# Optimization experiments

Measured on AMD Instinct MI355X. Metric: run time of the kernel, lower is better.

## Reference

```python
import jax, jax.numpy as jnp
import numpy as np

HID, FFN, E, K = 1024, 4096, 8, 2
CAP_FACTOR = 1.25


def setup_inputs() -> dict:
    key = jax.random.key(0)
    k1, k2, k3, k4 = jax.random.split(key, 4)
    B, T = 4, 2048
    x = jax.random.normal(k1, (B, T, HID), dtype=jnp.float32)
    router_w = jax.random.normal(k2, (E, HID), dtype=jnp.float32) * 0.02
    w1 = jax.random.normal(k3, (E, HID, FFN), dtype=jnp.float32) * 0.02
    w2 = jax.random.normal(k4, (E, FFN, HID), dtype=jnp.float32) * 0.02
    return {"x": x, "router_w": router_w, "w1": w1, "w2": w2}


def reference(x, router_w, w1, w2):
    B, T, H = x.shape
    N = B * T
    x_flat = x.reshape(N, H)
    # capacity per expert (static, shape-derived)
    C = max(1, int(CAP_FACTOR * N / E * K))

    # router (eval mode: no noise)
    logits = x_flat @ router_w.T                      # [N, E]
    probs = jax.nn.softmax(logits, axis=-1)
    top_v, top_i = jax.lax.top_k(probs, K)            # [N, K]
    top_v = top_v / jnp.sum(top_v, axis=-1, keepdims=True)

    out = jnp.zeros_like(x_flat)
    for k in range(K):
        eid = top_i[:, k]                             # [N] expert id per token
        gate = top_v[:, k]                            # [N]
        # position of each token within its expert, in token order
        onehot = jax.nn.one_hot(eid, E, dtype=jnp.int32)          # [N, E]
        pos = jnp.take_along_axis(jnp.cumsum(onehot, axis=0), eid[:, None], axis=1)[:, 0] - 1
        keep = pos < C                                # capacity drop (first C in token order)
        slot = jnp.where(keep, eid * C + pos, E * C)  # dropped tokens -> dump slot

        # dispatch: scatter kept tokens into per-expert capacity buffers
        buf = jnp.zeros((E * C + 1, H), dtype=x.dtype).at[slot].add(
            x_flat * keep[:, None].astype(x.dtype))
        expert_in = buf[: E * C].reshape(E, C, H)     # [E, C, H]

        # per-expert FFN (grouped GEMM -> GELU -> grouped GEMM)
        h = jax.nn.gelu(jnp.einsum('ech,ehf->ecf', expert_in, w1), approximate=False)
        y = jnp.einsum('ecf,efh->ech', h, w2)         # [E, C, H]

        # combine: gather back to token order, mask dropped, apply gate
        tok = y.reshape(E * C, H)[jnp.minimum(slot, E * C - 1)]
        out = out + tok * (gate * keep.astype(x.dtype))[:, None]

    return out.reshape(B, T, H)
```

## Files before the change

kernel.cpp:

```cpp
#include <hip/hip_runtime.h>
#include <hip/hip_bf16.h>
#include <math.h>

#define N_TOK 8192
#define HIDD  1024
#define FFND  4096
#define NE    8
#define CAP   2560
#define TMX   20
#define RMAX  16512

typedef __attribute__((ext_vector_type(4))) float  f32x4;
typedef __attribute__((ext_vector_type(8))) __bf16 bf16x8;

__device__ __forceinline__ unsigned short f2bf(float f) {
    unsigned u = __float_as_uint(f);
    u = (u + 0x7fffu + ((u >> 16) & 1u)) >> 16;
    return (unsigned short)u;
}

__device__ __forceinline__ void gld_lds16(const void* g, void* l) {
    __builtin_amdgcn_global_load_lds(
        (const __attribute__((address_space(1))) unsigned int*)g,
        (__attribute__((address_space(3))) unsigned int*)l, 16, 0, 0);
}

template <int R, int C>
__global__ __launch_bounds__(256) void transpose_cvt(const float* __restrict__ W,
                                                     unsigned short* __restrict__ Wt) {
    __shared__ unsigned short st[64][72];
    int e  = blockIdx.z;
    int r0 = blockIdx.y * 64, c0 = blockIdx.x * 64;
    int tid = threadIdx.x;
    int rb = tid >> 4, cq = tid & 15;
    const float* src = W + ((size_t)e * R + r0) * C + c0;
#pragma unroll
    for (int i = 0; i < 4; i++) {
        int kr = i * 16 + rb;
        float4 v = *reinterpret_cast<const float4*>(src + (size_t)kr * C + cq * 4);
        st[cq * 4 + 0][kr] = f2bf(v.x);
        st[cq * 4 + 1][kr] = f2bf(v.y);
        st[cq * 4 + 2][kr] = f2bf(v.z);
        st[cq * 4 + 3][kr] = f2bf(v.w);
    }
    __syncthreads();
    unsigned short* dst = Wt + ((size_t)e * C + c0) * R + r0;
#pragma unroll
    for (int i = 0; i < 4; i++) {
        int cr = i * 16 + rb;
        uint2 v = *reinterpret_cast<const uint2*>(&st[cr][cq * 4]);
        *reinterpret_cast<uint2*>(dst + (size_t)cr * R + cq * 4) = v;
    }
}

__global__ __launch_bounds__(256) void router_kernel(const float* __restrict__ x,
                                                     const float* __restrict__ rw,
                                                     unsigned short* __restrict__ xbf,
                                                     int* __restrict__ cnt,
                                                     int* __restrict__ tok,
                                                     float* __restrict__ gate) {
    __shared__ float4 rwl[2048];
    __shared__ int   e0s[32], e1s[32];
    __shared__ float g0s[32], g1s[32];
    __shared__ int   baseS[16];

    int tid = threadIdx.x, lane = tid & 63, w = tid >> 6;
    for (int i = tid; i < 2048; i += 256) rwl[i] = reinterpret_cast<const float4*>(rw)[i];
    __syncthreads();

    int tbase = blockIdx.x * 32 + w * 8;
    for (int i = 0; i < 8; i++) {
        int t = tbase + i;
        const float4* xr = reinterpret_cast<const float4*>(x) + (size_t)t * 256;
        float4 xv[4];
#pragma unroll
        for (int c = 0; c < 4; c++) xv[c] = xr[c * 64 + lane];
        uint2* xb = reinterpret_cast<uint2*>(xbf) + (size_t)t * 256;
#pragma unroll
        for (int c = 0; c < 4; c++) {
            uint2 p;
            p.x = (unsigned)f2bf(xv[c].x) | ((unsigned)f2bf(xv[c].y) << 16);
            p.y = (unsigned)f2bf(xv[c].z) | ((unsigned)f2bf(xv[c].w) << 16);
            xb[c * 64 + lane] = p;
        }
        float dot[NE];
#pragma unroll
        for (int e = 0; e < NE; e++) {
            float s = 0.f;
#pragma unroll
            for (int c = 0; c < 4; c++) {
                float4 a = rwl[e * 256 + c * 64 + lane];
                s += xv[c].x * a.x + xv[c].y * a.y + xv[c].z * a.z + xv[c].w * a.w;
            }
            dot[e] = s;
        }
#pragma unroll
        for (int e = 0; e < NE; e++) {
            float v = dot[e];
#pragma unroll
            for (int o = 32; o > 0; o >>= 1) v += __shfl_xor(v, o, 64);
            dot[e] = v;
        }
        if (lane == 0) {
            int e0 = 0; float l0 = dot[0];
#pragma unroll
            for (int e = 1; e < NE; e++) if (dot[e] > l0) { l0 = dot[e]; e0 = e; }
            int e1 = -1; float l1 = -3.4e38f;
#pragma unroll
            for (int e = 0; e < NE; e++) if (e != e0 && dot[e] > l1) { l1 = dot[e]; e1 = e; }
            float g0 = 1.f / (1.f + expf(l1 - l0));
            int j = w * 8 + i;
            e0s[j] = e0; e1s[j] = e1; g0s[j] = g0; g1s[j] = 1.f - g0;
        }
    }
    __syncthreads();

    int e0 = 255, e1 = 255, rank0 = 0, rank1 = 0, slotcnt = 0;
    float g0 = 0.f, g1 = 0.f;
    if (w == 0) {
        if (lane < 32) { e0 = e0s[lane]; e1 = e1s[lane]; g0 = g0s[lane]; g1 = g1s[lane]; }
        unsigned long long lt = (1ull << lane) - 1ull;
#pragma unroll
        for (int ee = 0; ee < NE; ee++) {
            unsigned long long m0 = __ballot(e0 == ee);
            unsigned long long m1 = __ballot(e1 == ee);
            if (e0 == ee) rank0 = (int)__popcll(m0 & lt);
            if (e1 == ee) rank1 = (int)__popcll(m1 & lt);
            if (lane == ee)      slotcnt = (int)__popcll(m0);
            if (lane == NE + ee) slotcnt = (int)__popcll(m1);
        }
        if (lane < 16) baseS[lane] = atomicAdd(&cnt[lane * 16], slotcnt);
    }
    __syncthreads();
    if (w == 0 && lane < 32) {
        int t = blockIdx.x * 32 + lane;
        int p0 = baseS[e0] + rank0;
        if (p0 < CAP) { tok[e0 * CAP + p0] = t; gate[e0 * CAP + p0] = g0; }
        int p1 = baseS[NE + e1] + rank1;
        if (p1 < CAP) { tok[(NE + e1) * CAP + p1] = t; gate[(NE + e1) * CAP + p1] = g1; }
    }
}

template <int KD, int ND, int KS, bool G1>
__global__ __launch_bounds__(512, 2) void ffn_gemm8(const unsigned short* __restrict__ A,
                                                    const unsigned short* __restrict__ Bw,
                                                    unsigned short* __restrict__ H,
                                                    float* __restrict__ O,
                                                    const int* __restrict__ cntAll,
                                                    const int* __restrict__ tokL,
                                                    const float* __restrict__ gateL) {
    constexpr int TN    = ND / 128;
    constexpr int UNITS = TN * KS;
    constexpr int CH    = G1 ? 8 : 4;
    constexpr int KDS   = KD / KS;
    constexpr int NT    = KDS / 64;
    constexpr int LDSA  = 256 * 128;
    constexpr int LDSB  = 128 * 128;
    constexpr int BUF   = LDSA + LDSB;

    extern __shared__ __align__(16) char smem[];

    int e = blockIdx.x & 7;
    int i = blockIdx.x >> 3;
    int cnt0 = min(cntAll[e * 16], CAP);
    int cnt1 = min(cntAll[(e + 8) * 16], CAP);
    int tmx0 = (cnt0 + 255) >> 8, tmx1 = (cnt1 + 255) >> 8;
    int tmsum = tmx0 + tmx1;
    if (tmsum == 0) return;
    int per_chunk = tmsum * CH;
    int c = i / per_chunk;
    if (c >= UNITS / CH) return;
    int r = i - c * per_chunk;
    int s, tm, cnt_e;
    if (r < tmx0 * CH) { s = e;     tm = r / CH; r -= tm * CH; cnt_e = cnt0; }
    else { r -= tmx0 * CH; s = e + 8; tm = r / CH; r -= tm * CH; cnt_e = cnt1; }
    int u  = c * CH + r;
    int tn = (KS > 1) ? (u / KS) : u;
    int ks = (KS > 1) ? (u % KS) : 0;

    int off_e = 0;
#pragma unroll
    for (int t = 0; t < 16; t++) off_e += (t < s) ? min(cntAll[t * 16], CAP) : 0;
    const int lbase = s * CAP;

    int tid = threadIdx.x;
    int l = tid & 63, w = tid >> 6;

    int srow = w * 8 + (l >> 3);
    int swz  = (((l & 7) ^ ((l >> 3) & 7)) << 4);

    int aoff[4];
#pragma unroll
    for (int j = 0; j < 4; j++) {
        int p = tm * 256 + j * 64 + srow;
        if (G1) {
            int t = tokL[lbase + (p < cnt_e ? p : 0)];
            aoff[j] = t * (KD * 2) + ks * (KDS * 2) + swz;
        } else {
            aoff[j] = (off_e + p) * (KD * 2) + ks * (KDS * 2) + swz;
        }
    }
    int boff[2];
#pragma unroll
    for (int j = 0; j < 2; j++) {
        int nr = e * ND + tn * 128 + j * 64 + srow;
        boff[j] = nr * (KD * 2) + ks * (KDS * 2) + swz;
    }
    int adst = w * 1024;

    const char* Ab = (const char*)A;
    const char* Bb = (const char*)Bw;

    int wm = w >> 1, wn = w & 1;
    int arow = wm * 64 + (l & 15);
    int brow = wn * 64 + (l & 15);
    int rsw  = (((l >> 4) ^ (l & 7)) << 4);
    int aR0 = arow * 128 + rsw;
    int bR0 = brow * 128 + rsw;

    f32x4 acc[4][4];
#pragma unroll
    for (int m = 0; m < 4; m++)
#pragma unroll
        for (int n = 0; n < 4; n++) acc[m][n] = (f32x4){0.f, 0.f, 0.f, 0.f};

    char* b0 = smem;
    char* b1 = smem + BUF;
    char* b2 = smem + 2 * BUF;

#define STAGE_A(buf) do { _Pragma("unroll") \
    for (int j = 0; j < 4; j++) { gld_lds16(Ab + aoff[j], (buf) + adst + j * 8192); aoff[j] += 128; } } while (0)
#define STAGE_B(buf) do { _Pragma("unroll") \
    for (int j = 0; j < 2; j++) { gld_lds16(Bb + boff[j], (buf) + LDSA + adst + j * 8192); boff[j] += 128; } } while (0)

    STAGE_A(b0); STAGE_B(b0);
    STAGE_A(b1); STAGE_B(b1);
    asm volatile("s_waitcnt vmcnt(6)" ::: "memory");
    __builtin_amdgcn_s_barrier();
    asm volatile("" ::: "memory");

    for (int t = 0; t < NT; t++) {
        bool pf = (t + 2 < NT);
        bf16x8 af[4], bf[4];
#pragma unroll
        for (int m = 0; m < 4; m++) af[m] = *reinterpret_cast<const bf16x8*>(b0 + aR0 + m * 2048);
#pragma unroll
        for (int n = 0; n < 4; n++) bf[n] = *reinterpret_cast<const bf16x8*>(b0 + LDSA + bR0 + n * 2048);
        if (pf) STAGE_A(b2);
        __builtin_amdgcn_s_setprio(1);
#pragma unroll
        for (int m = 0; m < 4; m++)
#pragma unroll
            for (int n = 0; n < 4; n++)
                acc[m][n] = __builtin_amdgcn_mfma_f32_16x16x32_bf16(af[m], bf[n], acc[m][n], 0, 0, 0);
        __builtin_amdgcn_s_setprio(0);
#pragma unroll
        for (int m = 0; m < 4; m++) af[m] = *reinterpret_cast<const bf16x8*>(b0 + (aR0 ^ 64) + m * 2048);
#pragma unroll
        for (int n = 0; n < 4; n++) bf[n] = *reinterpret_cast<const bf16x8*>(b0 + LDSA + (bR0 ^ 64) + n * 2048);
        if (pf) STAGE_B(b2);
        __builtin_amdgcn_s_setprio(1);
#pragma unroll
        for (int m = 0; m < 4; m++)
#pragma unroll
            for (int n = 0; n < 4; n++)
                acc[m][n] = __builtin_amdgcn_mfma_f32_16x16x32_bf16(af[m], bf[n], acc[m][n], 0, 0, 0);
        __builtin_amdgcn_s_setprio(0);
        if (pf) asm volatile("s_waitcnt vmcnt(6)" ::: "memory");
        else    asm volatile("s_waitcnt vmcnt(0)" ::: "memory");
        if (t + 1 < NT) {
            __builtin_amdgcn_s_barrier();
            asm volatile("" ::: "memory");
        }
        char* bt = b0; b0 = b1; b1 = b2; b2 = bt;
    }
#undef STAGE_A
#undef STAGE_B

    if (G1) {
#pragma unroll
        for (int m = 0; m < 4; m++) {
#pragma unroll
            for (int j = 0; j < 4; j++) {
                int rr = wm * 64 + m * 16 + (l >> 4) * 4 + j;
                int p = tm * 256 + rr;
                if (p < cnt_e) {
                    unsigned short* hp = H + (size_t)(off_e + p) * ND + tn * 128 + wn * 64 + (l & 15);
#pragma unroll
                    for (int n = 0; n < 4; n++) {
                        float v = acc[m][n][j];
                        float g = 0.5f * v * (1.f + erff(v * 0.70710678118654752f));
                        hp[n * 16] = f2bf(g);
                    }
                }
            }
        }
    } else {
#pragma unroll
        for (int m = 0; m < 4; m++) {
#pragma unroll
            for (int j = 0; j < 4; j++) {
                int rr = wm * 64 + m * 16 + (l >> 4) * 4 + j;
                int p = tm * 256 + rr;
                if (p < cnt_e) {
                    int t = tokL[lbase + p];
                    float gv = gateL[lbase + p];
                    float* op = O + (size_t)t * ND + tn * 128 + wn * 64 + (l & 15);
#pragma unroll
                    for (int n = 0; n < 4; n++) atomicAdd(op + n * 16, gv * acc[m][n][j]);
                }
            }
        }
    }
}

template <int KD, int ND, bool G1>
__global__ __launch_bounds__(256) void ffn_gemm(const unsigned short* __restrict__ A,
                                                const float* __restrict__ W,
                                                unsigned short* __restrict__ H,
                                                float* __restrict__ O,
                                                const int* __restrict__ cntAll,
                                                const int* __restrict__ tokL,
                                                const float* __restrict__ gateL,
                                                int slot0, int pbase) {
    constexpr int TN = ND / 128;
    int bid = blockIdx.x;
    int tn  = bid % TN;
    int tme = bid / TN;
    int tm  = tme % TMX;
    int s   = slot0 + tme / TMX;
    int eW  = s & 7;
    int cnt_e = min(cntAll[s * 16], CAP);
    if (tm * 128 >= cnt_e) return;
    int off_e = 0;
#pragma unroll
    for (int i = 0; i < 16; i++) {
        int c = min(cntAll[i * 16], CAP);
        off_e += (i >= pbase && i < s) ? c : 0;
    }
    const int lbase = s * CAP;

    __shared__ __align__(16) unsigned short At[128 * 32];
    __shared__ __align__(16) unsigned short Bt[128 * 32];

    int tid = threadIdx.x;
    int w = tid >> 6, l = tid & 63;
    int wr = w >> 1, wc = w & 1;

    int r1 = tid >> 2, q1 = tid & 3;
    int r2 = r1 + 64;
    const char* aSrc1;
    const char* aSrc2;
    if (G1) {
        int p1 = tm * 128 + r1, p2 = tm * 128 + r2;
        int t1 = tokL[lbase + (p1 < cnt_e ? p1 : 0)];
        int t2 = tokL[lbase + (p2 < cnt_e ? p2 : 0)];
        aSrc1 = (const char*)(A + (size_t)t1 * KD) + ((q1 ^ ((r1 >> 1) & 3)) << 4);
        aSrc2 = (const char*)(A + (size_t)t2 * KD) + ((q1 ^ ((r2 >> 1) & 3)) << 4);
    } else {
        size_t row1 = (size_t)off_e + tm * 128 + r1;
        size_t row2 = row1 + 64;
        aSrc1 = (const char*)(A + row1 * KD) + ((q1 ^ ((r1 >> 1) & 3)) << 4);
        aSrc2 = (const char*)(A + row2 * KD) + ((q1 ^ ((r2 >> 1) & 3)) << 4);
    }
    char* aDst1 = (char*)At + w * 1024;
    char* aDst2 = aDst1 + 4096;

    const float* bSrc[4];
    int bOff[16];
#pragma unroll
    for (int j = 0; j < 4; j++) {
        int fidx = j * 1024 + tid * 4;
        int kk = fidx >> 7, n = fidx & 127;
        bSrc[j] = W + (size_t)eW * KD * ND + (size_t)kk * ND + tn * 128 + n;
#pragma unroll
        for (int i = 0; i < 4; i++) {
            int nn = n + i;
            bOff[j * 4 + i] = nn * 64 + ((((kk >> 3) ^ ((nn >> 1) & 3))) << 4) + ((kk & 7) << 1);
        }
    }

    int aro[4], bro[4];
#pragma unroll
    for (int m = 0; m < 4; m++) {
        int rr = wr * 64 + m * 16 + (l & 15);
        aro[m] = rr * 64 + (((l >> 4) ^ ((rr >> 1) & 3)) << 4);
        int cc = wc * 64 + m * 16 + (l & 15);
        bro[m] = cc * 64 + (((l >> 4) ^ ((cc >> 1) & 3)) << 4);
    }

    f32x4 zf = {0.f, 0.f, 0.f, 0.f};
    f32x4 acc[4][4];
#pragma unroll
    for (int m = 0; m < 4; m++)
#pragma unroll
        for (int n = 0; n < 4; n++) acc[m][n] = zf;

    for (int k0 = 0; k0 < KD; k0 += 32) {
        gld_lds16(aSrc1 + (size_t)k0 * 2, aDst1);
        gld_lds16(aSrc2 + (size_t)k0 * 2, aDst2);
        float4 bv[4];
#pragma unroll
        for (int j = 0; j < 4; j++) bv[j] = *reinterpret_cast<const float4*>(bSrc[j] + (size_t)k0 * ND);
        char* btc = (char*)Bt;
#pragma unroll
        for (int j = 0; j < 4; j++) {
            *(unsigned short*)(btc + bOff[j * 4 + 0]) = f2bf(bv[j].x);
            *(unsigned short*)(btc + bOff[j * 4 + 1]) = f2bf(bv[j].y);
            *(unsigned short*)(btc + bOff[j * 4 + 2]) = f2bf(bv[j].z);
            *(unsigned short*)(btc + bOff[j * 4 + 3]) = f2bf(bv[j].w);
        }
        __syncthreads();
        bf16x8 af[4], bf[4];
#pragma unroll
        for (int m = 0; m < 4; m++) af[m] = *reinterpret_cast<const bf16x8*>((const char*)At + aro[m]);
#pragma unroll
        for (int n = 0; n < 4; n++) bf[n] = *reinterpret_cast<const bf16x8*>((const char*)Bt + bro[n]);
#pragma unroll
        for (int m = 0; m < 4; m++)
#pragma unroll
            for (int n = 0; n < 4; n++)
                acc[m][n] = __builtin_amdgcn_mfma_f32_16x16x32_bf16(af[m], bf[n], acc[m][n], 0, 0, 0);
        __syncthreads();
    }

    if (G1) {
#pragma unroll
        for (int m = 0; m < 4; m++) {
#pragma unroll
            for (int j = 0; j < 4; j++) {
                int rr = wr * 64 + m * 16 + (l >> 4) * 4 + j;
                int p = tm * 128 + rr;
                if (p < cnt_e) {
                    size_t row = (size_t)(off_e + p);
                    unsigned short* hp = H + row * ND + tn * 128 + wc * 64 + (l & 15);
#pragma unroll
                    for (int n = 0; n < 4; n++) {
                        float v = acc[m][n][j];
                        float g = 0.5f * v * (1.f + erff(v * 0.70710678118654752f));
                        hp[n * 16] = f2bf(g);
                    }
                }
            }
        }
    } else {
#pragma unroll
        for (int m = 0; m < 4; m++) {
#pragma unroll
            for (int j = 0; j < 4; j++) {
                int rr = wr * 64 + m * 16 + (l >> 4) * 4 + j;
                int p = tm * 128 + rr;
                if (p < cnt_e) {
                    int t = tokL[lbase + p];
                    float gv = gateL[lbase + p];
                    float* op = O + (size_t)t * ND + tn * 128 + wc * 64 + (l & 15);
#pragma unroll
                    for (int n = 0; n < 4; n++) atomicAdd(op + n * 16, gv * acc[m][n][j]);
                }
            }
        }
    }
}

extern "C" void kernel_launch(void* const* d_in, const int* in_sizes, int n_in,
                              void* d_out, int out_size, void* d_ws, size_t ws_size,
                              hipStream_t stream) {
    const float* x  = (const float*)d_in[0];
    const float* rw = (const float*)d_in[1];
    const float* w1 = (const float*)d_in[2];
    const float* w2 = (const float*)d_in[3];
    float* out = (float*)d_out;
    char* ws = (char*)d_ws;

    int*   cnt  = (int*)ws;
    int*   tok  = (int*)(ws + 4096);
    float* gate = (float*)(ws + 4096 + 16 * CAP * 4);
    unsigned short* xbf = (unsigned short*)(ws + (1 << 20));
    size_t hOff = (1 << 20) + (size_t)N_TOK * HIDD * 2;
    unsigned short* h = (unsigned short*)(ws + hOff);

    size_t w1tSz = (size_t)NE * HIDD * FFND * 2;
    size_t hBig = (size_t)RMAX * FFND * 2;
    size_t needBig = hOff + hBig + 2 * w1tSz;

    hipMemsetAsync(cnt, 0, 1024, stream);
    hipMemsetAsync(d_out, 0, (size_t)N_TOK * HIDD * 4, stream);

    hipLaunchKernelGGL(router_kernel, dim3(N_TOK / 32), dim3(256), 0, stream,
                       x, rw, xbf, cnt, tok, gate);

    if (ws_size >= needBig) {
        unsigned short* w1t = (unsigned short*)(ws + hOff + hBig);
        unsigned short* w2t = (unsigned short*)(ws + hOff + hBig + w1tSz);
        hipLaunchKernelGGL((transpose_cvt<HIDD, FFND>), dim3(FFND / 64, HIDD / 64, NE), dim3(256), 0, stream, w1, w1t);
        hipLaunchKernelGGL((transpose_cvt<FFND, HIDD>), dim3(HIDD / 64, FFND / 64, NE), dim3(256), 0, stream, w2, w2t);
        constexpr int SMEM = 3 * (256 * 128 + 128 * 128);
        hipLaunchKernelGGL((ffn_gemm8<HIDD, FFND, 1, true>), dim3(8 * 20 * 32), dim3(512),
                           SMEM, stream, xbf, w1t, h, (float*)nullptr, cnt, tok, gate);
        hipLaunchKernelGGL((ffn_gemm8<FFND, HIDD, 2, false>), dim3(8 * 20 * 16), dim3(512),
                           SMEM, stream, h, w2t, (unsigned short*)nullptr, out, cnt, tok, gate);
    } else {
        for (int k = 0; k < 2; k++) {
            hipLaunchKernelGGL((ffn_gemm<HIDD, FFND, true>), dim3(8 * TMX * (FFND / 128)), dim3(256), 0, stream,
                               xbf, w1, h, (float*)nullptr, cnt, tok, gate, 8 * k, 8 * k);
            hipLaunchKernelGGL((ffn_gemm<FFND, HIDD, false>), dim3(8 * TMX * (HIDD / 128)), dim3(256), 0, stream,
                               h, w2, (unsigned short*)nullptr, out, cnt, tok, gate, 8 * k, 8 * k);
        }
    }
}
```

Before: 572.1 us.

## Switch expert GEMMs to 256x256 tiles with four-stage LDS pipeline

Replaces the 256x128 tile, 3-buffer GEMM with a 256x256 output tile per block, K-step 32, and a 4-deep ring of 32 KB LDS buffers, with each wave computing 128x64 (8x4 MFMA accumulators). This raises arithmetic intensity per LDS byte and halves the number of B-tile reloads, while the deeper prefetch is meant to better hide global-to-LDS latency. It costs more barriers per iteration, doubles accumulator registers, and drops occupancy to one block per CU with 128 KB of LDS.

```diff
diff --git a/kernel.cpp b/kernel.cpp
--- a/kernel.cpp
+++ b/kernel.cpp
@@ -8,6 +8,7 @@
 #define NE    8
 #define CAP   2560
 #define TMX   20
+#define TMX4  10
 #define RMAX  16512
 
 typedef __attribute__((ext_vector_type(4))) float  f32x4;
@@ -142,21 +143,19 @@
 }
 
 template <int KD, int ND, int KS, bool G1>
-__global__ __launch_bounds__(512, 2) void ffn_gemm8(const unsigned short* __restrict__ A,
-                                                    const unsigned short* __restrict__ Bw,
-                                                    unsigned short* __restrict__ H,
-                                                    float* __restrict__ O,
-                                                    const int* __restrict__ cntAll,
-                                                    const int* __restrict__ tokL,
-                                                    const float* __restrict__ gateL) {
-    constexpr int TN    = ND / 128;
+__global__ __launch_bounds__(512, 1) void ffn_gemm4p(const unsigned short* __restrict__ A,
+                                                     const unsigned short* __restrict__ Bw,
+                                                     unsigned short* __restrict__ H,
+                                                     float* __restrict__ O,
+                                                     const int* __restrict__ cntAll,
+                                                     const int* __restrict__ tokL,
+                                                     const float* __restrict__ gateL) {
+    constexpr int TN    = ND / 256;
     constexpr int UNITS = TN * KS;
-    constexpr int CH    = G1 ? 8 : 4;
+    constexpr int CH    = 4;
     constexpr int KDS   = KD / KS;
-    constexpr int NT    = KDS / 64;
-    constexpr int LDSA  = 256 * 128;
-    constexpr int LDSB  = 128 * 128;
-    constexpr int BUF   = LDSA + LDSB;
+    constexpr int NT    = KDS / 32;
+    constexpr int BUFSZ = 32768;
 
     extern __shared__ __align__(16) char smem[];
 
@@ -186,67 +185,63 @@
     int tid = threadIdx.x;
     int l = tid & 63, w = tid >> 6;
 
-    int srow = w * 8 + (l >> 3);
-    int swz  = (((l & 7) ^ ((l >> 3) & 7)) << 4);
-
-    int aoff[4];
-#pragma unroll
-    for (int j = 0; j < 4; j++) {
-        int p = tm * 256 + j * 64 + srow;
+    int rowi   = w * 16 + (l >> 2);
+    int schunk = (((l & 3) ^ ((l >> 3) & 3)) << 4);
+
+    int aoff[2], boff[2];
+#pragma unroll
+    for (int j = 0; j < 2; j++) {
+        int p = tm * 256 + j * 128 + rowi;
         if (G1) {
             int t = tokL[lbase + (p < cnt_e ? p : 0)];
-            aoff[j] = t * (KD * 2) + ks * (KDS * 2) + swz;
+            aoff[j] = t * (KD * 2) + ks * (KDS * 2) + schunk;
         } else {
-            aoff[j] = (off_e + p) * (KD * 2) + ks * (KDS * 2) + swz;
-        }
-    }
-    int boff[2];
-#pragma unroll
-    for (int j = 0; j < 2; j++) {
-        int nr = e * ND + tn * 128 + j * 64 + srow;
-        boff[j] = nr * (KD * 2) + ks * (KDS * 2) + swz;
-    }
-    int adst = w * 1024;
+            aoff[j] = (off_e + p) * (KD * 2) + ks * (KDS * 2) + schunk;
+        }
+        int nr = e * ND + tn * 256 + j * 128 + rowi;
+        boff[j] = nr * (KD * 2) + ks * (KDS * 2) + schunk;
+    }
+    int dstw = w * 1024;
 
     const char* Ab = (const char*)A;
     const char* Bb = (const char*)Bw;
 
-    int wm = w >> 1, wn = w & 1;
-    int arow = wm * 64 + (l & 15);
-    int brow = wn * 64 + (l & 15);
-    int rsw  = (((l >> 4) ^ (l & 7)) << 4);
-    int aR0 = arow * 128 + rsw;
-    int bR0 = brow * 128 + rsw;
-
-    f32x4 acc[4][4];
-#pragma unroll
-    for (int m = 0; m < 4; m++)
+    int wm = w >> 2, wn = w & 3;
+    int rswz = (((l >> 4) ^ ((l >> 1) & 3)) << 4);
+    int aRd = (wm * 128 + (l & 15)) * 64 + rswz;
+    int bRd = (wn * 64 + (l & 15)) * 64 + rswz + 16384;
+
+    f32x4 acc[8][4];
+#pragma unroll
+    for (int m = 0; m < 8; m++)
 #pragma unroll
         for (int n = 0; n < 4; n++) acc[m][n] = (f32x4){0.f, 0.f, 0.f, 0.f};
 
-    char* b0 = smem;
-    char* b1 = smem + BUF;
-    char* b2 = smem + 2 * BUF;
-
-#define STAGE_A(buf) do { _Pragma("unroll") \
-    for (int j = 0; j < 4; j++) { gld_lds16(Ab + aoff[j], (buf) + adst + j * 8192); aoff[j] += 128; } } while (0)
-#define STAGE_B(buf) do { _Pragma("unroll") \
-    for (int j = 0; j < 2; j++) { gld_lds16(Bb + boff[j], (buf) + LDSA + adst + j * 8192); boff[j] += 128; } } while (0)
-
-    STAGE_A(b0); STAGE_B(b0);
-    STAGE_A(b1); STAGE_B(b1);
-    asm volatile("s_waitcnt vmcnt(6)" ::: "memory");
+#define STAGE_A4(bb) do { _Pragma("unroll") \
+    for (int j = 0; j < 2; j++) { gld_lds16(Ab + aoff[j], smem + (bb) + j * 8192 + dstw); aoff[j] += 64; } } while (0)
+#define STAGE_B4(bb) do { _Pragma("unroll") \
+    for (int j = 0; j < 2; j++) { gld_lds16(Bb + boff[j], smem + (bb) + 16384 + j * 8192 + dstw); boff[j] += 64; } } while (0)
+
+#pragma unroll
+    for (int t = 0; t < 3; t++) { STAGE_A4(t * BUFSZ); STAGE_B4(t * BUFSZ); }
+    asm volatile("s_waitcnt vmcnt(8)" ::: "memory");
     __builtin_amdgcn_s_barrier();
     asm volatile("" ::: "memory");
 
     for (int t = 0; t < NT; t++) {
-        bool pf = (t + 2 < NT);
+        const int cb = (t & 3) * BUFSZ;
+        const int nb = ((t + 3) & 3) * BUFSZ;
+        bool pf = (t + 3) < NT;
         bf16x8 af[4], bf[4];
 #pragma unroll
-        for (int m = 0; m < 4; m++) af[m] = *reinterpret_cast<const bf16x8*>(b0 + aR0 + m * 2048);
-#pragma unroll
-        for (int n = 0; n < 4; n++) bf[n] = *reinterpret_cast<const bf16x8*>(b0 + LDSA + bR0 + n * 2048);
-        if (pf) STAGE_A(b2);
+        for (int n = 0; n < 4; n++) bf[n] = *reinterpret_cast<const bf16x8*>(smem + cb + bRd + n * 1024);
+#pragma unroll
+        for (int m = 0; m < 4; m++) af[m] = *reinterpret_cast<const bf16x8*>(smem + cb + aRd + m * 1024);
+        if (pf) STAGE_A4(nb);
+        __builtin_amdgcn_s_barrier();
+        asm volatile("" ::: "memory");
+        asm volatile("s_waitcnt lgkmcnt(0)" ::: "memory");
+        __builtin_amdgcn_sched_barrier(0);
         __builtin_amdgcn_s_setprio(1);
 #pragma unroll
         for (int m = 0; m < 4; m++)
@@ -254,38 +249,40 @@
             for (int n = 0; n < 4; n++)
                 acc[m][n] = __builtin_amdgcn_mfma_f32_16x16x32_bf16(af[m], bf[n], acc[m][n], 0, 0, 0);
         __builtin_amdgcn_s_setprio(0);
-#pragma unroll
-        for (int m = 0; m < 4; m++) af[m] = *reinterpret_cast<const bf16x8*>(b0 + (aR0 ^ 64) + m * 2048);
-#pragma unroll
-        for (int n = 0; n < 4; n++) bf[n] = *reinterpret_cast<const bf16x8*>(b0 + LDSA + (bR0 ^ 64) + n * 2048);
-        if (pf) STAGE_B(b2);
+        __builtin_amdgcn_s_barrier();
+        asm volatile("" ::: "memory");
+#pragma unroll
+        for (int m = 0; m < 4; m++) af[m] = *reinterpret_cast<const bf16x8*>(smem + cb + aRd + (m + 4) * 1024);
+        if (pf) STAGE_B4(nb);
+        if (t + 3 < NT)      asm volatile("s_waitcnt vmcnt(8)" ::: "memory");
+        else if (t + 2 < NT) asm volatile("s_waitcnt vmcnt(4)" ::: "memory");
+        else if (t + 1 < NT) asm volatile("s_waitcnt vmcnt(0)" ::: "memory");
+        __builtin_amdgcn_s_barrier();
+        asm volatile("" ::: "memory");
+        asm volatile("s_waitcnt lgkmcnt(0)" ::: "memory");
+        __builtin_amdgcn_sched_barrier(0);
         __builtin_amdgcn_s_setprio(1);
 #pragma unroll
         for (int m = 0; m < 4; m++)
 #pragma unroll
             for (int n = 0; n < 4; n++)
-                acc[m][n] = __builtin_amdgcn_mfma_f32_16x16x32_bf16(af[m], bf[n], acc[m][n], 0, 0, 0);
+                acc[m + 4][n] = __builtin_amdgcn_mfma_f32_16x16x32_bf16(af[m], bf[n], acc[m + 4][n], 0, 0, 0);
         __builtin_amdgcn_s_setprio(0);
-        if (pf) asm volatile("s_waitcnt vmcnt(6)" ::: "memory");
-        else    asm volatile("s_waitcnt vmcnt(0)" ::: "memory");
-        if (t + 1 < NT) {
-            __builtin_amdgcn_s_barrier();
-            asm volatile("" ::: "memory");
-        }
-        char* bt = b0; b0 = b1; b1 = b2; b2 = bt;
-    }
-#undef STAGE_A
-#undef STAGE_B
+        __builtin_amdgcn_s_barrier();
+        asm volatile("" ::: "memory");
+    }
+#undef STAGE_A4
+#undef STAGE_B4
 
     if (G1) {
 #pragma unroll
-        for (int m = 0; m < 4; m++) {
+        for (int m = 0; m < 8; m++) {
 #pragma unroll
             for (int j = 0; j < 4; j++) {
-                int rr = wm * 64 + m * 16 + (l >> 4) * 4 + j;
+                int rr = wm * 128 + m * 16 + (l >> 4) * 4 + j;
                 int p = tm * 256 + rr;
                 if (p < cnt_e) {
-                    unsigned short* hp = H + (size_t)(off_e + p) * ND + tn * 128 + wn * 64 + (l & 15);
+                    unsigned short* hp = H + (size_t)(off_e + p) * ND + tn * 256 + wn * 64 + (l & 15);
 #pragma unroll
                     for (int n = 0; n < 4; n++) {
                         float v = acc[m][n][j];
@@ -297,15 +294,15 @@
         }
     } else {
 #pragma unroll
-        for (int m = 0; m < 4; m++) {
+        for (int m = 0; m < 8; m++) {
 #pragma unroll
             for (int j = 0; j < 4; j++) {
-                int rr = wm * 64 + m * 16 + (l >> 4) * 4 + j;
+                int rr = wm * 128 + m * 16 + (l >> 4) * 4 + j;
                 int p = tm * 256 + rr;
                 if (p < cnt_e) {
                     int t = tokL[lbase + p];
                     float gv = gateL[lbase + p];
-                    float* op = O + (size_t)t * ND + tn * 128 + wn * 64 + (l & 15);
+                    float* op = O + (size_t)t * ND + tn * 256 + wn * 64 + (l & 15);
 #pragma unroll
                     for (int n = 0; n < 4; n++) atomicAdd(op + n * 16, gv * acc[m][n][j]);
                 }
@@ -494,10 +491,10 @@
         unsigned short* w2t = (unsigned short*)(ws + hOff + hBig + w1tSz);
         hipLaunchKernelGGL((transpose_cvt<HIDD, FFND>), dim3(FFND / 64, HIDD / 64, NE), dim3(256), 0, stream, w1, w1t);
         hipLaunchKernelGGL((transpose_cvt<FFND, HIDD>), dim3(HIDD / 64, FFND / 64, NE), dim3(256), 0, stream, w2, w2t);
-        constexpr int SMEM = 3 * (256 * 128 + 128 * 128);
-        hipLaunchKernelGGL((ffn_gemm8<HIDD, FFND, 1, true>), dim3(8 * 20 * 32), dim3(512),
+        constexpr int SMEM = 4 * 32768;
+        hipLaunchKernelGGL((ffn_gemm4p<HIDD, FFND, 1, true>), dim3(8 * 2 * TMX4 * 16), dim3(512),
                            SMEM, stream, xbf, w1t, h, (float*)nullptr, cnt, tok, gate);
-        hipLaunchKernelGGL((ffn_gemm8<FFND, HIDD, 2, false>), dim3(8 * 20 * 16), dim3(512),
+        hipLaunchKernelGGL((ffn_gemm4p<FFND, HIDD, 2, false>), dim3(8 * 2 * TMX4 * 8), dim3(512),
                            SMEM, stream, h, w2t, (unsigned short*)nullptr, out, cnt, tok, gate);
     } else {
         for (int k = 0; k < 2; k++) {
```

Result: slower. 604.4 us (+5.6%).
